# Performance work log

Measured on AMD Instinct MI355X. Metric: run time of the kernel, lower is better.

## Reference

```python
import jax, jax.numpy as jnp
import numpy as np

B, C, H, W = 2, 256, 96, 96
KC = 32  # key_channels


def setup_inputs() -> dict:
    key = jax.random.key(0)
    ks = jax.random.split(key, 10)
    s_in = 1.0 / np.sqrt(C)
    s_kc = 1.0 / np.sqrt(KC)
    return {
        "x": jax.random.normal(ks[0], (B, C, H, W), jnp.float32),
        "human": jax.random.normal(ks[1], (B, C, H, W), jnp.float32),
        "Wq": jax.random.normal(ks[2], (KC, C), jnp.float32) * s_in,
        "bq": jnp.zeros((KC,), jnp.float32),
        "Wd": jax.random.normal(ks[3], (KC, C), jnp.float32) * s_in,
        "bd": jnp.zeros((KC,), jnp.float32),
        "Wf": jax.random.normal(ks[4], (KC, KC), jnp.float32) * s_kc,
        "bf": jnp.zeros((KC,), jnp.float32),
        "Wu": jax.random.normal(ks[5], (C, KC), jnp.float32) * s_kc,
        "bu": jnp.zeros((C,), jnp.float32),
    }


def reference(x, human, Wq, bq, Wd, bd, Wf, bf, Wu, bu):
    b, c, h, w = x.shape
    kc = Wq.shape[0]
    n = h * w
    # 1x1 conv projections == per-pixel matmul
    q = (jnp.einsum('bchw,kc->bkhw', human, Wq) + bq[None, :, None, None]).reshape(b, kc, n)
    # sim_map = scale * q^T q over spatial positions, softmax over last dim
    sim = jnp.einsum('bkn,bkm->bnm', q, q) * (kc ** -0.5)  # (b, n, n)
    sim = jax.nn.softmax(sim, axis=-1)
    v = (jnp.einsum('bchw,kc->bkhw', x, Wd) + bd[None, :, None, None]).reshape(b, kc, n)
    # context[b, n, k] = sim @ v^T  -> back to (b, kc, h, w)
    ctx = jnp.einsum('bnm,bkm->bkn', sim, v).reshape(b, kc, h, w)
    # f: 1x1 conv + bias + ReLU (ConvModule default act)
    ctx = jax.nn.relu(jnp.einsum('bkhw,jk->bjhw', ctx, Wf) + bf[None, :, None, None])
    # f_up: 1x1 conv + bias, no activation (act_cfg=None)
    ctx = jnp.einsum('bkhw,ck->bchw', ctx, Wu) + bu[None, :, None, None]
    return x + ctx
```

## Files before the change

### kernel.cpp

```cpp
#include <hip/hip_runtime.h>
#include <hip/hip_bf16.h>

#define NB 2
#define CCH 256
#define NPIX 9216
#define KCH 32
#define NTILE 288
#define SQSCALE 0.5050098f

#define QPA_B 73728u
#define VBS_B 294912u

typedef __attribute__((ext_vector_type(8)))  short short8;
typedef __attribute__((ext_vector_type(16))) float f32x16;
typedef __attribute__((ext_vector_type(4)))  unsigned uint4v;

union ABu { unsigned u[4]; uint4v v4; short8 s; };

__device__ __forceinline__ unsigned pk2(float a, float b) {
  __hip_bfloat162 h = __float22bfloat162_rn(make_float2(a, b));
  unsigned r; __builtin_memcpy(&r, &h, 4); return r;
}
__device__ __forceinline__ unsigned short bf1(float a) {
  __hip_bfloat16 h = __float2bfloat16(a);
  unsigned short r; __builtin_memcpy(&r, &h, 2); return r;
}
__device__ __forceinline__ float bfx(unsigned short h) {
  unsigned v = ((unsigned)h) << 16;
  float f; __builtin_memcpy(&f, &v, 4); return f;
}
__device__ __forceinline__ void split_pk(float a, float b, unsigned &hp, unsigned &lp) {
  unsigned short ha = bf1(a), hb_ = bf1(b);
  hp = (unsigned)ha | ((unsigned)hb_ << 16);
  unsigned short la = bf1(a - bfx(ha)), lb = bf1(b - bfx(hb_));
  lp = (unsigned)la | ((unsigned)lb << 16);
}
__device__ __forceinline__ void plswap(unsigned &a, unsigned &b) {
  auto r = __builtin_amdgcn_permlane32_swap(a, b, false, false);
  a = r[0]; b = r[1];
}

#define MFMA32(a, b, c) __builtin_amdgcn_mfma_f32_32x32x16_bf16((a), (b), (c), 0, 0, 0)

__global__ __launch_bounds__(256) void proj_mfma(
    const float* __restrict__ x, const float* __restrict__ human,
    const float* __restrict__ Wq, const float* __restrict__ bq,
    const float* __restrict__ Wd, const float* __restrict__ bd,
    unsigned* __restrict__ qPA,
    unsigned* __restrict__ qPB,
    unsigned short* __restrict__ vBS)
{
  __shared__ float4 slab[4][8][64];
  const int tid = threadIdx.x;
  const int w   = tid >> 6;
  const int l   = tid & 63;
  const int hi  = l >> 5;
  const int ql  = l & 31;
  const int blk = blockIdx.x;
  const int b   = blk / NTILE;
  const int tN  = blk % NTILE;
  const int n0  = tN * 32;
  const int c0  = w * 64;
  const float* hb = human + (size_t)b*CCH*NPIX;
  const float* xb = x + (size_t)b*CCH*NPIX;

  ABu aqh[4], aqlo[4], adh[4], adlo[4];
#pragma unroll
  for (int s = 0; s < 4; ++s) {
    const int cbase = c0 + 16*s + 8*hi;
#pragma unroll
    for (int j = 0; j < 4; ++j) {
      const float q0 = Wq[ql*CCH + cbase + 2*j], q1 = Wq[ql*CCH + cbase + 2*j + 1];
      const float d0 = Wd[ql*CCH + cbase + 2*j], d1 = Wd[ql*CCH + cbase + 2*j + 1];
      split_pk(q0, q1, aqh[s].u[j], aqlo[s].u[j]);
      split_pk(d0, d1, adh[s].u[j], adlo[s].u[j]);
    }
  }

  f32x16 qa, va;
#pragma unroll
  for (int r = 0; r < 16; ++r) { qa[r] = 0.f; va[r] = 0.f; }

#pragma unroll
  for (int s = 0; s < 4; ++s) {
    const int cbase = c0 + 16*s + 8*hi;
    ABu bhh, bhl, bxh, bxl;
#pragma unroll
    for (int j = 0; j < 4; ++j) {
      const float h0 = hb[(size_t)(cbase + 2*j  )*NPIX + n0 + ql];
      const float h1 = hb[(size_t)(cbase + 2*j+1)*NPIX + n0 + ql];
      const float x0 = xb[(size_t)(cbase + 2*j  )*NPIX + n0 + ql];
      const float x1 = xb[(size_t)(cbase + 2*j+1)*NPIX + n0 + ql];
      split_pk(h0, h1, bhh.u[j], bhl.u[j]);
      split_pk(x0, x1, bxh.u[j], bxl.u[j]);
    }
    qa = MFMA32(aqh[s].s,  bhh.s, qa);
    qa = MFMA32(aqh[s].s,  bhl.s, qa);
    qa = MFMA32(aqlo[s].s, bhh.s, qa);
    va = MFMA32(adh[s].s,  bxh.s, va);
    va = MFMA32(adh[s].s,  bxl.s, va);
    va = MFMA32(adlo[s].s, bxh.s, va);
  }

#pragma unroll
  for (int jf = 0; jf < 4; ++jf) {
    slab[w][jf  ][l] = make_float4(qa[4*jf], qa[4*jf+1], qa[4*jf+2], qa[4*jf+3]);
    slab[w][4+jf][l] = make_float4(va[4*jf], va[4*jf+1], va[4*jf+2], va[4*jf+3]);
  }
  __syncthreads();
  if (w == 0) {
    unsigned* qpa = qPA + (size_t)b*QPA_B;
    unsigned* qpb = qPB + (size_t)b*QPA_B;
    unsigned short* vbs = vBS + (size_t)b*VBS_B;
#pragma unroll
    for (int jf = 0; jf < 4; ++jf) {
      const int kc = 8*jf + 4*hi;
      float4 s0 = slab[0][jf][l], s1 = slab[1][jf][l], s2 = slab[2][jf][l], s3 = slab[3][jf][l];
      const float v0 = (s0.x+s1.x+s2.x+s3.x + bq[kc+0]) * SQSCALE;
      const float v1 = (s0.y+s1.y+s2.y+s3.y + bq[kc+1]) * SQSCALE;
      const float v2 = (s0.z+s1.z+s2.z+s3.z + bq[kc+2]) * SQSCALE;
      const float v3 = (s0.w+s1.w+s2.w+s3.w + bq[kc+3]) * SQSCALE;
      const int p0 = 4*jf + 2*hi;
      unsigned* a0p = (p0 < 8) ? qpa : qpb;
      a0p[(size_t)tN*256 + ((p0&7)>>2)*128 + ql*4 + (p0&3)] = pk2(v0, v1);
      const int p1 = p0 + 1;
      unsigned* a1p = (p1 < 8) ? qpa : qpb;
      a1p[(size_t)tN*256 + ((p1&7)>>2)*128 + ql*4 + (p1&3)] = pk2(v2, v3);
      float4 t0 = slab[0][4+jf][l], t1 = slab[1][4+jf][l], t2 = slab[2][4+jf][l], t3 = slab[3][4+jf][l];
      const size_t vbase = (size_t)tN*1024 + (size_t)(ql>>4)*512 + (size_t)(ql&15);
      vbs[vbase + (size_t)(kc+0)*16] = bf1(t0.x+t1.x+t2.x+t3.x + bd[kc+0]);
      vbs[vbase + (size_t)(kc+1)*16] = bf1(t0.y+t1.y+t2.y+t3.y + bd[kc+1]);
      vbs[vbase + (size_t)(kc+2)*16] = bf1(t0.z+t1.z+t2.z+t3.z + bd[kc+2]);
      vbs[vbase + (size_t)(kc+3)*16] = bf1(t0.w+t1.w+t2.w+t3.w + bd[kc+3]);
    }
  }
}

__global__ __launch_bounds__(64, 4) void attn_wave(
    const unsigned* __restrict__ qPA, const unsigned* __restrict__ qPB,
    const unsigned short* __restrict__ vBS,
    float4* __restrict__ pO4,
    float* __restrict__ pL)
{
  const int l   = threadIdx.x;
  const int hi  = l >> 5;
  const int ql  = l & 31;
  const int blk = blockIdx.x;
  const int swz = (blk & 7)*576 + (blk >> 3);
  const int b   = swz / 2304;
  const int r2  = swz % 2304;
  const int qt  = r2 >> 4;
  const int ks  = r2 & 15;

  const unsigned* qa_ = qPA + (size_t)b*QPA_B;
  const unsigned* qb_ = qPB + (size_t)b*QPA_B;
  const unsigned short* vb_ = vBS + (size_t)b*VBS_B;

  ABu bqA1, bqA2, bqB1, bqB2;
  bqA1.v4 = *(const uint4v*)(qa_ + (size_t)(2*qt  )*256 + hi*128 + ql*4);
  bqA2.v4 = *(const uint4v*)(qb_ + (size_t)(2*qt  )*256 + hi*128 + ql*4);
  bqB1.v4 = *(const uint4v*)(qa_ + (size_t)(2*qt+1)*256 + hi*128 + ql*4);
  bqB2.v4 = *(const uint4v*)(qb_ + (size_t)(2*qt+1)*256 + hi*128 + ql*4);

  f32x16 OA, OB, Z;
#pragma unroll
  for (int r = 0; r < 16; ++r) { OA[r] = 0.f; OB[r] = 0.f; Z[r] = 0.f; }
  float lsA = 0.f, lsB = 0.f;

  for (int it = 0; it < 18; ++it) {
    const int t = ks*18 + it;
    const size_t ko = (size_t)t*256 + hi*128 + ql*4;
    ABu ak1, ak2;
    ak1.v4 = *(const uint4v*)(qa_ + ko);
    ak2.v4 = *(const uint4v*)(qb_ + ko);
    const size_t vo = (size_t)t*1024 + (size_t)ql*16 + hi*8;
    const short8 av1 = *(const short8*)(vb_ + vo);
    const short8 av2 = *(const short8*)(vb_ + vo + 512);

    f32x16 s = MFMA32(ak1.s, bqA1.s, Z);
    s = MFMA32(ak2.s, bqA2.s, s);
    float p[16];
#pragma unroll
    for (int r = 0; r < 16; ++r) p[r] = __builtin_amdgcn_exp2f(s[r]);
    lsA += (((p[0]+p[1])+(p[2]+p[3])) + ((p[4]+p[5])+(p[6]+p[7])))
         + (((p[8]+p[9])+(p[10]+p[11])) + ((p[12]+p[13])+(p[14]+p[15])));
    {
      unsigned a0 = pk2(p[0],p[1]),  a1 = pk2(p[2],p[3]);
      unsigned b0 = pk2(p[4],p[5]),  b1 = pk2(p[6],p[7]);
      unsigned a2 = pk2(p[8],p[9]),  a3 = pk2(p[10],p[11]);
      unsigned b2 = pk2(p[12],p[13]),b3 = pk2(p[14],p[15]);
      plswap(a0,b0); plswap(a1,b1); plswap(a2,b2); plswap(a3,b3);
      ABu pb1, pb2;
      pb1.u[0]=a0; pb1.u[1]=a1; pb1.u[2]=b0; pb1.u[3]=b1;
      pb2.u[0]=a2; pb2.u[1]=a3; pb2.u[2]=b2; pb2.u[3]=b3;
      OA = MFMA32(av1, pb1.s, OA);
      OA = MFMA32(av2, pb2.s, OA);
    }
    s = MFMA32(ak1.s, bqB1.s, Z);
    s = MFMA32(ak2.s, bqB2.s, s);
#pragma unroll
    for (int r = 0; r < 16; ++r) p[r] = __builtin_amdgcn_exp2f(s[r]);
    lsB += (((p[0]+p[1])+(p[2]+p[3])) + ((p[4]+p[5])+(p[6]+p[7])))
         + (((p[8]+p[9])+(p[10]+p[11])) + ((p[12]+p[13])+(p[14]+p[15])));
    {
      unsigned a0 = pk2(p[0],p[1]),  a1 = pk2(p[2],p[3]);
      unsigned b0 = pk2(p[4],p[5]),  b1 = pk2(p[6],p[7]);
      unsigned a2 = pk2(p[8],p[9]),  a3 = pk2(p[10],p[11]);
      unsigned b2 = pk2(p[12],p[13]),b3 = pk2(p[14],p[15]);
      plswap(a0,b0); plswap(a1,b1); plswap(a2,b2); plswap(a3,b3);
      ABu pb1, pb2;
      pb1.u[0]=a0; pb1.u[1]=a1; pb1.u[2]=b0; pb1.u[3]=b1;
      pb2.u[0]=a2; pb2.u[1]=a3; pb2.u[2]=b2; pb2.u[3]=b3;
      OB = MFMA32(av1, pb1.s, OB);
      OB = MFMA32(av2, pb2.s, OB);
    }
  }

  lsA += __shfl_xor(lsA, 32);
  lsB += __shfl_xor(lsB, 32);
#pragma unroll
  for (int rq = 0; rq < 4; ++rq) {
    pO4[((size_t)swz*8 + rq    )*64 + l] = make_float4(OA[4*rq], OA[4*rq+1], OA[4*rq+2], OA[4*rq+3]);
    pO4[((size_t)swz*8 + 4 + rq)*64 + l] = make_float4(OB[4*rq], OB[4*rq+1], OB[4*rq+2], OB[4*rq+3]);
  }
  if (l < 32) {
    pL[(size_t)swz*64 + l]      = lsA;
    pL[(size_t)swz*64 + 32 + l] = lsB;
  }
}

__global__ __launch_bounds__(64) void attn_merge(
    const float4* __restrict__ pO4, const float* __restrict__ pL,
    float* __restrict__ ctx)
{
  const int l   = threadIdx.x;
  const int blk = blockIdx.x;
  const int b   = blk / 576;
  const int rem = blk % 576;
  const int qt  = rem >> 2;
  const int kcq = rem & 3;
  const int f   = l >> 5;
  const int qlm = l & 31;

  float ax=0,ay=0,az=0,aw=0, bx=0,by=0,bz=0,bw=0, L=0;
  const size_t base = (size_t)b*2304 + (size_t)qt*16;
#pragma unroll 4
  for (int ks = 0; ks < 16; ++ks) {
    const size_t pb_ = base + ks;
    const float4* pp = pO4 + (pb_*8 + (size_t)f*4 + kcq)*64;
    const float4 t0 = pp[qlm];
    const float4 t1 = pp[qlm + 32];
    ax += t0.x; ay += t0.y; az += t0.z; aw += t0.w;
    bx += t1.x; by += t1.y; bz += t1.z; bw += t1.w;
    L  += pL[pb_*64 + l];
  }
  const float inv = 1.f / L;
  float* cb = ctx + ((size_t)b*KCH + kcq*8)*NPIX + (size_t)qt*64 + l;
  cb[0*NPIX] = ax*inv;  cb[1*NPIX] = ay*inv;
  cb[2*NPIX] = az*inv;  cb[3*NPIX] = aw*inv;
  cb[4*NPIX] = bx*inv;  cb[5*NPIX] = by*inv;
  cb[6*NPIX] = bz*inv;  cb[7*NPIX] = bw*inv;
}

__global__ __launch_bounds__(512, 6) void attn_mfma(
    const unsigned* __restrict__ qPA, const unsigned* __restrict__ qPB,
    const unsigned short* __restrict__ vBS,
    float* __restrict__ ctx)
{
  __shared__ float slab[8][32][32];
  __shared__ float mlbuf[8][32];
  const int tid = threadIdx.x;
  const int w   = tid >> 6;
  const int l   = tid & 63;
  const int hi  = l >> 5;
  const int ql  = l & 31;
  const int blk = blockIdx.x;
  const int b   = blk / NTILE;
  const int tq  = blk % NTILE;
  const int q0  = tq * 32;

  const unsigned* qa_ = qPA + (size_t)b*QPA_B;
  const unsigned* qb_ = qPB + (size_t)b*QPA_B;
  const unsigned short* vb_ = vBS + (size_t)b*VBS_B;

  ABu bq1, bq2;
  bq1.v4 = *(const uint4v*)(qa_ + (size_t)tq*256 + hi*128 + ql*4);
  bq2.v4 = *(const uint4v*)(qb_ + (size_t)tq*256 + hi*128 + ql*4);

  f32x16 O;
#pragma unroll
  for (int r = 0; r < 16; ++r) O[r] = 0.f;
  float lsum = 0.f;

  for (int it = 0; it < 36; ++it) {
    const int t = it*8 + w;
    const size_t ko = (size_t)t*256 + hi*128 + ql*4;
    ABu ak1, ak2;
    ak1.v4 = *(const uint4v*)(qa_ + ko);
    ak2.v4 = *(const uint4v*)(qb_ + ko);
    const size_t vo = (size_t)t*1024 + (size_t)ql*16 + hi*8;
    const short8 av1 = *(const short8*)(vb_ + vo);
    const short8 av2 = *(const short8*)(vb_ + vo + 512);

    f32x16 s;
#pragma unroll
    for (int r = 0; r < 16; ++r) s[r] = 0.f;
    s = MFMA32(ak1.s, bq1.s, s);
    s = MFMA32(ak2.s, bq2.s, s);

    float p[16];
#pragma unroll
    for (int r = 0; r < 16; ++r) p[r] = __builtin_amdgcn_exp2f(s[r]);
    lsum += (((p[0]+p[1])+(p[2]+p[3])) + ((p[4]+p[5])+(p[6]+p[7])))
          + (((p[8]+p[9])+(p[10]+p[11])) + ((p[12]+p[13])+(p[14]+p[15])));

    unsigned a0 = pk2(p[0],p[1]),  a1 = pk2(p[2],p[3]);
    unsigned b0 = pk2(p[4],p[5]),  b1 = pk2(p[6],p[7]);
    unsigned a2 = pk2(p[8],p[9]),  a3 = pk2(p[10],p[11]);
    unsigned b2 = pk2(p[12],p[13]),b3 = pk2(p[14],p[15]);
    plswap(a0,b0); plswap(a1,b1); plswap(a2,b2); plswap(a3,b3);
    ABu pb1, pb2;
    pb1.u[0]=a0; pb1.u[1]=a1; pb1.u[2]=b0; pb1.u[3]=b1;
    pb2.u[0]=a2; pb2.u[1]=a3; pb2.u[2]=b2; pb2.u[3]=b3;

    O = MFMA32(av1, pb1.s, O);
    O = MFMA32(av2, pb2.s, O);
  }

  lsum += __shfl_xor(lsum, 32);
  if (hi == 0) mlbuf[w][ql] = lsum;
#pragma unroll
  for (int r = 0; r < 16; ++r)
    slab[w][(r&3) + 8*(r>>2) + 4*hi][ql] = O[r];
  __syncthreads();

  {
    const int q  = tid & 31;
    const int kh = tid >> 5;
    float L = 0.f;
#pragma unroll
    for (int ww = 0; ww < 8; ++ww) L += mlbuf[ww][q];
    const float inv = 1.f / L;
#pragma unroll
    for (int i = 0; i < 2; ++i) {
      const int kc = kh + 16*i;
      float acc = 0.f;
#pragma unroll
      for (int ww = 0; ww < 8; ++ww) acc += slab[ww][kc][q];
      ctx[((size_t)b*KCH + kc)*NPIX + q0 + q] = acc * inv;
    }
  }
}

__global__ __launch_bounds__(64) void epi_kernel8(
    const float* __restrict__ x, const float* __restrict__ ctx,
    const float* __restrict__ Wf, const float* __restrict__ bf,
    const float* __restrict__ Wu, const float* __restrict__ bu,
    float* __restrict__ out)
{
  __shared__ float4 swf[256];
  __shared__ float4 swu[256];
  const int lane = threadIdx.x;
  const int blk = blockIdx.x;
  const int pb = blk % 288;
  const int co = blk / 288;
  const int b = pb / 144;
  const int n = (pb % 144)*64 + lane;
#pragma unroll
  for (int it = 0; it < 4; ++it) swf[it*64 + lane] = ((const float4*)Wf)[it*64 + lane];
#pragma unroll
  for (int it = 0; it < 4; ++it) swu[it*64 + lane] = ((const float4*)Wu)[co*256 + it*64 + lane];
  __syncthreads();
  const float* cb = ctx + (size_t)b*KCH*NPIX + n;
  float cv[KCH];
#pragma unroll
  for (int k = 0; k < KCH; ++k) cv[k] = cb[(size_t)k*NPIX];
  float gv[KCH];
#pragma unroll
  for (int j = 0; j < KCH; ++j) {
    float acc = bf[j];
#pragma unroll
    for (int w = 0; w < 8; ++w) {
      const float4 wv = swf[j*8 + w];
      acc += wv.x*cv[4*w+0] + wv.y*cv[4*w+1] + wv.z*cv[4*w+2] + wv.w*cv[4*w+3];
    }
    gv[j] = fmaxf(acc, 0.f);
  }
  const float* xb = x + ((size_t)b*CCH + co*32)*NPIX + n;
  float* ob = out + ((size_t)b*CCH + co*32)*NPIX + n;
#pragma unroll 4
  for (int c = 0; c < 32; ++c) {
    float acc = bu[co*32 + c];
#pragma unroll
    for (int w = 0; w < 8; ++w) {
      const float4 wv = swu[c*8 + w];
      acc += wv.x*gv[4*w+0] + wv.y*gv[4*w+1] + wv.z*gv[4*w+2] + wv.w*gv[4*w+3];
    }
    ob[(size_t)c*NPIX] = xb[(size_t)c*NPIX] + acc;
  }
}

extern "C" void kernel_launch(void* const* d_in, const int* in_sizes, int n_in,
                              void* d_out, int out_size, void* d_ws, size_t ws_size,
                              hipStream_t stream) {
  (void)in_sizes; (void)n_in; (void)out_size;
  const float* x     = (const float*)d_in[0];
  const float* human = (const float*)d_in[1];
  const float* Wq    = (const float*)d_in[2];
  const float* bq    = (const float*)d_in[3];
  const float* Wd    = (const float*)d_in[4];
  const float* bd    = (const float*)d_in[5];
  const float* Wf    = (const float*)d_in[6];
  const float* bf    = (const float*)d_in[7];
  const float* Wu    = (const float*)d_in[8];
  const float* bu    = (const float*)d_in[9];
  float* out = (float*)d_out;

  unsigned* qPA       = (unsigned*)d_ws;
  unsigned* qPB       = qPA + (size_t)NB*QPA_B;
  unsigned short* vBS = (unsigned short*)(qPB + (size_t)NB*QPA_B);
  float* ctx          = (float*)(vBS + (size_t)NB*VBS_B);
  float4* pO4         = (float4*)(ctx + (size_t)NB*KCH*NPIX);
  float* pL           = (float*)(pO4 + (size_t)4608*8*64);

  const size_t need = ((char*)(pL + (size_t)4608*64)) - (char*)d_ws;

  proj_mfma<<<576, 256, 0, stream>>>(x, human, Wq, bq, Wd, bd, qPA, qPB, vBS);
  if (ws_size >= need) {
    attn_wave<<<4608, 64, 0, stream>>>(qPA, qPB, vBS, pO4, pL);
    attn_merge<<<1152, 64, 0, stream>>>(pO4, pL, ctx);
  } else {
    attn_mfma<<<576, 512, 0, stream>>>(qPA, qPB, vBS, ctx);
  }
  epi_kernel8<<<2304, 64, 0, stream>>>(x, ctx, Wf, bf, Wu, bu, out);
}
```

Before: 181.5 us.

## Split epilogue into pixel-major g kernel and wider up-projection, double proj waves

The context tensor is now stored pixel-major so each pixel's 32 channels load as contiguous float4s. The Wf+ReLU stage moves into its own g_kernel instead of being recomputed by all eight channel-group blocks in the old epilogue. The up-projection kernel now runs four waves per block over 16 output channels each. The projection kernel also uses 512 threads with half the channel range per wave, for more parallelism during the loads. The cost is an extra launch and a global round trip for the intermediate g tensor.

New measurement: 177.4 us. 2.3% less time.

```diff
diff --git a/kernel.cpp b/kernel.cpp
--- a/kernel.cpp
+++ b/kernel.cpp
@@ -42,7 +42,7 @@
 
 #define MFMA32(a, b, c) __builtin_amdgcn_mfma_f32_32x32x16_bf16((a), (b), (c), 0, 0, 0)
 
-__global__ __launch_bounds__(256) void proj_mfma(
+__global__ __launch_bounds__(512, 4) void proj_mfma(
     const float* __restrict__ x, const float* __restrict__ human,
     const float* __restrict__ Wq, const float* __restrict__ bq,
     const float* __restrict__ Wd, const float* __restrict__ bd,
@@ -50,7 +50,7 @@
     unsigned* __restrict__ qPB,
     unsigned short* __restrict__ vBS)
 {
-  __shared__ float4 slab[4][8][64];
+  __shared__ float4 slab[8][8][64];
   const int tid = threadIdx.x;
   const int w   = tid >> 6;
   const int l   = tid & 63;
@@ -60,13 +60,13 @@
   const int b   = blk / NTILE;
   const int tN  = blk % NTILE;
   const int n0  = tN * 32;
-  const int c0  = w * 64;
+  const int c0  = w * 32;
   const float* hb = human + (size_t)b*CCH*NPIX;
   const float* xb = x + (size_t)b*CCH*NPIX;
 
-  ABu aqh[4], aqlo[4], adh[4], adlo[4];
-#pragma unroll
-  for (int s = 0; s < 4; ++s) {
+  ABu aqh[2], aqlo[2], adh[2], adlo[2];
+#pragma unroll
+  for (int s = 0; s < 2; ++s) {
     const int cbase = c0 + 16*s + 8*hi;
 #pragma unroll
     for (int j = 0; j < 4; ++j) {
@@ -82,7 +82,7 @@
   for (int r = 0; r < 16; ++r) { qa[r] = 0.f; va[r] = 0.f; }
 
 #pragma unroll
-  for (int s = 0; s < 4; ++s) {
+  for (int s = 0; s < 2; ++s) {
     const int cbase = c0 + 16*s + 8*hi;
     ABu bhh, bhl, bxh, bxl;
 #pragma unroll
@@ -115,23 +115,29 @@
 #pragma unroll
     for (int jf = 0; jf < 4; ++jf) {
       const int kc = 8*jf + 4*hi;
-      float4 s0 = slab[0][jf][l], s1 = slab[1][jf][l], s2 = slab[2][jf][l], s3 = slab[3][jf][l];
-      const float v0 = (s0.x+s1.x+s2.x+s3.x + bq[kc+0]) * SQSCALE;
-      const float v1 = (s0.y+s1.y+s2.y+s3.y + bq[kc+1]) * SQSCALE;
-      const float v2 = (s0.z+s1.z+s2.z+s3.z + bq[kc+2]) * SQSCALE;
-      const float v3 = (s0.w+s1.w+s2.w+s3.w + bq[kc+3]) * SQSCALE;
+      float sx=0, sy=0, sz=0, sw=0, tx=0, ty=0, tz=0, tw=0;
+#pragma unroll
+      for (int ww = 0; ww < 8; ++ww) {
+        const float4 sq = slab[ww][jf][l];
+        const float4 tv = slab[ww][4+jf][l];
+        sx += sq.x; sy += sq.y; sz += sq.z; sw += sq.w;
+        tx += tv.x; ty += tv.y; tz += tv.z; tw += tv.w;
+      }
+      const float v0 = (sx + bq[kc+0]) * SQSCALE;
+      const float v1 = (sy + bq[kc+1]) * SQSCALE;
+      const float v2 = (sz + bq[kc+2]) * SQSCALE;
+      const float v3 = (sw + bq[kc+3]) * SQSCALE;
       const int p0 = 4*jf + 2*hi;
       unsigned* a0p = (p0 < 8) ? qpa : qpb;
       a0p[(size_t)tN*256 + ((p0&7)>>2)*128 + ql*4 + (p0&3)] = pk2(v0, v1);
       const int p1 = p0 + 1;
       unsigned* a1p = (p1 < 8) ? qpa : qpb;
       a1p[(size_t)tN*256 + ((p1&7)>>2)*128 + ql*4 + (p1&3)] = pk2(v2, v3);
-      float4 t0 = slab[0][4+jf][l], t1 = slab[1][4+jf][l], t2 = slab[2][4+jf][l], t3 = slab[3][4+jf][l];
       const size_t vbase = (size_t)tN*1024 + (size_t)(ql>>4)*512 + (size_t)(ql&15);
-      vbs[vbase + (size_t)(kc+0)*16] = bf1(t0.x+t1.x+t2.x+t3.x + bd[kc+0]);
-      vbs[vbase + (size_t)(kc+1)*16] = bf1(t0.y+t1.y+t2.y+t3.y + bd[kc+1]);
-      vbs[vbase + (size_t)(kc+2)*16] = bf1(t0.z+t1.z+t2.z+t3.z + bd[kc+2]);
-      vbs[vbase + (size_t)(kc+3)*16] = bf1(t0.w+t1.w+t2.w+t3.w + bd[kc+3]);
+      vbs[vbase + (size_t)(kc+0)*16] = bf1(tx + bd[kc+0]);
+      vbs[vbase + (size_t)(kc+1)*16] = bf1(ty + bd[kc+1]);
+      vbs[vbase + (size_t)(kc+2)*16] = bf1(tz + bd[kc+2]);
+      vbs[vbase + (size_t)(kc+3)*16] = bf1(tw + bd[kc+3]);
     }
   }
 }
@@ -231,7 +237,7 @@
 
 __global__ __launch_bounds__(64) void attn_merge(
     const float4* __restrict__ pO4, const float* __restrict__ pL,
-    float* __restrict__ ctx)
+    float* __restrict__ ctxP)
 {
   const int l   = threadIdx.x;
   const int blk = blockIdx.x;
@@ -255,17 +261,15 @@
     L  += pL[pb_*64 + l];
   }
   const float inv = 1.f / L;
-  float* cb = ctx + ((size_t)b*KCH + kcq*8)*NPIX + (size_t)qt*64 + l;
-  cb[0*NPIX] = ax*inv;  cb[1*NPIX] = ay*inv;
-  cb[2*NPIX] = az*inv;  cb[3*NPIX] = aw*inv;
-  cb[4*NPIX] = bx*inv;  cb[5*NPIX] = by*inv;
-  cb[6*NPIX] = bz*inv;  cb[7*NPIX] = bw*inv;
+  float* cp = ctxP + ((size_t)b*NPIX + (size_t)qt*64 + l)*32 + kcq*8;
+  ((float4*)cp)[0] = make_float4(ax*inv, ay*inv, az*inv, aw*inv);
+  ((float4*)cp)[1] = make_float4(bx*inv, by*inv, bz*inv, bw*inv);
 }
 
 __global__ __launch_bounds__(512, 6) void attn_mfma(
     const unsigned* __restrict__ qPA, const unsigned* __restrict__ qPB,
     const unsigned short* __restrict__ vBS,
-    float* __restrict__ ctx)
+    float* __restrict__ ctxP)
 {
   __shared__ float slab[8][32][32];
   __shared__ float mlbuf[8][32];
@@ -347,54 +351,85 @@
       float acc = 0.f;
 #pragma unroll
       for (int ww = 0; ww < 8; ++ww) acc += slab[ww][kc][q];
-      ctx[((size_t)b*KCH + kc)*NPIX + q0 + q] = acc * inv;
-    }
-  }
-}
-
-__global__ __launch_bounds__(64) void epi_kernel8(
-    const float* __restrict__ x, const float* __restrict__ ctx,
-    const float* __restrict__ Wf, const float* __restrict__ bf,
+      ctxP[((size_t)b*NPIX + q0 + q)*32 + kc] = acc * inv;
+    }
+  }
+}
+
+__global__ __launch_bounds__(256) void g_kernel(
+    const float* __restrict__ ctxP, const float* __restrict__ Wf,
+    const float* __restrict__ bf, float* __restrict__ gP)
+{
+  __shared__ float4 swf[256];
+  const int tid = threadIdx.x;
+  const int blk = blockIdx.x;
+  const int b   = blk / 144;
+  const int pg  = blk % 144;
+  swf[tid] = ((const float4*)Wf)[tid];
+  __syncthreads();
+  const int nl = tid >> 2;
+  const int cq = tid & 3;
+  const int n  = pg*64 + nl;
+  float cc[32];
+  const float4* cp = (const float4*)(ctxP + ((size_t)b*NPIX + n)*32);
+#pragma unroll
+  for (int i = 0; i < 8; ++i) {
+    const float4 t = cp[i];
+    cc[4*i] = t.x; cc[4*i+1] = t.y; cc[4*i+2] = t.z; cc[4*i+3] = t.w;
+  }
+  float r[8];
+#pragma unroll
+  for (int jj = 0; jj < 8; ++jj) {
+    const int j = cq*8 + jj;
+    float acc = bf[j];
+#pragma unroll
+    for (int k8 = 0; k8 < 8; ++k8) {
+      const float4 wv = swf[j*8 + k8];
+      acc += wv.x*cc[4*k8] + wv.y*cc[4*k8+1] + wv.z*cc[4*k8+2] + wv.w*cc[4*k8+3];
+    }
+    r[jj] = fmaxf(acc, 0.f);
+  }
+  float4* go = (float4*)(gP + ((size_t)b*NPIX + n)*32 + cq*8);
+  go[0] = make_float4(r[0], r[1], r[2], r[3]);
+  go[1] = make_float4(r[4], r[5], r[6], r[7]);
+}
+
+__global__ __launch_bounds__(256) void epi_v3(
+    const float* __restrict__ x, const float* __restrict__ gP,
     const float* __restrict__ Wu, const float* __restrict__ bu,
     float* __restrict__ out)
 {
-  __shared__ float4 swf[256];
-  __shared__ float4 swu[256];
-  const int lane = threadIdx.x;
-  const int blk = blockIdx.x;
-  const int pb = blk % 288;
-  const int co = blk / 288;
-  const int b = pb / 144;
-  const int n = (pb % 144)*64 + lane;
-#pragma unroll
-  for (int it = 0; it < 4; ++it) swf[it*64 + lane] = ((const float4*)Wf)[it*64 + lane];
-#pragma unroll
-  for (int it = 0; it < 4; ++it) swu[it*64 + lane] = ((const float4*)Wu)[co*256 + it*64 + lane];
+  __shared__ float4 swu[512];
+  const int tid = threadIdx.x;
+  const int w   = tid >> 6;
+  const int l   = tid & 63;
+  const int blk = blockIdx.x;
+  const int b   = blk / 576;
+  const int rem = blk % 576;
+  const int cquad = rem / 144;
+  const int pg  = rem % 144;
+  const int co  = cquad*4 + w;
+  const int n   = pg*64 + l;
+#pragma unroll
+  for (int it = 0; it < 2; ++it)
+    swu[it*256 + tid] = ((const float4*)Wu)[cquad*512 + it*256 + tid];
   __syncthreads();
-  const float* cb = ctx + (size_t)b*KCH*NPIX + n;
-  float cv[KCH];
-#pragma unroll
-  for (int k = 0; k < KCH; ++k) cv[k] = cb[(size_t)k*NPIX];
-  float gv[KCH];
-#pragma unroll
-  for (int j = 0; j < KCH; ++j) {
-    float acc = bf[j];
-#pragma unroll
-    for (int w = 0; w < 8; ++w) {
-      const float4 wv = swf[j*8 + w];
-      acc += wv.x*cv[4*w+0] + wv.y*cv[4*w+1] + wv.z*cv[4*w+2] + wv.w*cv[4*w+3];
-    }
-    gv[j] = fmaxf(acc, 0.f);
-  }
-  const float* xb = x + ((size_t)b*CCH + co*32)*NPIX + n;
-  float* ob = out + ((size_t)b*CCH + co*32)*NPIX + n;
-#pragma unroll 4
-  for (int c = 0; c < 32; ++c) {
-    float acc = bu[co*32 + c];
-#pragma unroll
-    for (int w = 0; w < 8; ++w) {
-      const float4 wv = swu[c*8 + w];
-      acc += wv.x*gv[4*w+0] + wv.y*gv[4*w+1] + wv.z*gv[4*w+2] + wv.w*gv[4*w+3];
+  float gg[32];
+  const float4* gp = (const float4*)(gP + ((size_t)b*NPIX + n)*32);
+#pragma unroll
+  for (int i = 0; i < 8; ++i) {
+    const float4 t = gp[i];
+    gg[4*i] = t.x; gg[4*i+1] = t.y; gg[4*i+2] = t.z; gg[4*i+3] = t.w;
+  }
+  const float* xb = x + ((size_t)b*CCH + co*16)*NPIX + n;
+  float* ob = out + ((size_t)b*CCH + co*16)*NPIX + n;
+#pragma unroll
+  for (int c = 0; c < 16; ++c) {
+    float acc = bu[co*16 + c];
+#pragma unroll
+    for (int j = 0; j < 8; ++j) {
+      const float4 wv = swu[(w*16 + c)*8 + j];
+      acc += wv.x*gg[4*j] + wv.y*gg[4*j+1] + wv.z*gg[4*j+2] + wv.w*gg[4*j+3];
     }
     ob[(size_t)c*NPIX] = xb[(size_t)c*NPIX] + acc;
   }
@@ -419,18 +454,20 @@
   unsigned* qPA       = (unsigned*)d_ws;
   unsigned* qPB       = qPA + (size_t)NB*QPA_B;
   unsigned short* vBS = (unsigned short*)(qPB + (size_t)NB*QPA_B);
-  float* ctx          = (float*)(vBS + (size_t)NB*VBS_B);
-  float4* pO4         = (float4*)(ctx + (size_t)NB*KCH*NPIX);
+  float* ctxP         = (float*)(vBS + (size_t)NB*VBS_B);
+  float* gP           = ctxP + (size_t)NB*NPIX*32;
+  float4* pO4         = (float4*)(gP + (size_t)NB*NPIX*32);
   float* pL           = (float*)(pO4 + (size_t)4608*8*64);
 
   const size_t need = ((char*)(pL + (size_t)4608*64)) - (char*)d_ws;
 
-  proj_mfma<<<576, 256, 0, stream>>>(x, human, Wq, bq, Wd, bd, qPA, qPB, vBS);
+  proj_mfma<<<576, 512, 0, stream>>>(x, human, Wq, bq, Wd, bd, qPA, qPB, vBS);
   if (ws_size >= need) {
     attn_wave<<<4608, 64, 0, stream>>>(qPA, qPB, vBS, pO4, pL);
-    attn_merge<<<1152, 64, 0, stream>>>(pO4, pL, ctx);
+    attn_merge<<<1152, 64, 0, stream>>>(pO4, pL, ctxP);
   } else {
-    attn_mfma<<<576, 512, 0, stream>>>(qPA, qPB, vBS, ctx);
-  }
-  epi_kernel8<<<2304, 64, 0, stream>>>(x, ctx, Wf, bf, Wu, bu, out);
-}
+    attn_mfma<<<576, 512, 0, stream>>>(qPA, qPB, vBS, ctxP);
+  }
+  g_kernel<<<288, 256, 0, stream>>>(ctxP, Wf, bf, gP);
+  epi_v3<<<1152, 256, 0, stream>>>(x, gP, Wu, bu, out);
+}
```
